# Optimization experiments

Hardware: AMD Instinct MI355X
Metric: run time of the kernel (lower is better)

The kernel has to match this reference:

```python
import jax, jax.numpy as jnp
import numpy as np
import math

EMBED_DIM = 512
B, H, W = 32, 56, 56


def gen_offsets(c):
    # Faithful port of SpiralFC.gen_offset. offset_groups == c (one (dy, dx) pair
    # per input channel). Only pairs 0..c//2-1 are written by the original code
    # (the loop over num_dims writes the same indices twice); the remaining pairs
    # come from torch.empty and are undefined -> we use 0 for determinism.
    dy = np.zeros(c, dtype=np.float32)
    dx = np.zeros(c, dtype=np.float32)
    num_dim = c // 2
    R = 14.0
    for i in range(num_dim):
        if i <= num_dim // 2:
            r = i * (R / num_dim)
        else:
            r = R - i * (R / num_dim)
        dy[i] = round(r * math.cos(math.pi * i / 16))  # torchvision offset order: (y, x)
        dx[i] = round(r * math.sin(math.pi * i / 16))
    return np.stack([dy, dx], axis=1)  # [C, 2]


def setup_inputs() -> dict:
    key = jax.random.key(0)
    k1, k2, k3 = jax.random.split(key, 3)
    C = EMBED_DIM
    fan_in = C  # 1x1 kernel, groups=1
    x = jax.random.normal(k1, (B, H, W, C), dtype=jnp.float32)
    weight = jax.random.normal(k2, (C, C), dtype=jnp.float32) / np.sqrt(fan_in)
    bias = (jax.random.uniform(k3, (C,), dtype=jnp.float32) - 0.5) * (2.0 / np.sqrt(fan_in))
    offset = jnp.asarray(gen_offsets(C))  # [C, 2] fixed buffer
    return {"x": x, "weight": weight, "bias": bias, "offset": offset}


def _shift_bilinear(xc, dy, dx):
    # xc: [B, C, H, W]; dy, dx: [C] spatially-constant per-channel offsets.
    # Bilinear sampling at (h + dy[c], w + dx[c]) with zero padding, separable
    # along H and W because offsets are constant over space.
    Bn, C, Hn, Wn = xc.shape

    def axis_interp(a, off, axis, size):
        p = jnp.arange(size, dtype=off.dtype)[None, :] + off[:, None]  # [C, size]
        p0 = jnp.floor(p)
        w1 = p - p0                      # [C, size]
        i0 = p0.astype(jnp.int32)
        i1 = i0 + 1

        def gather(idx):
            valid = (idx >= 0) & (idx < size)        # [C, size]
            idxc = jnp.clip(idx, 0, size - 1)
            if axis == 2:
                ind = idxc[None, :, :, None]
                msk = valid[None, :, :, None]
            else:
                ind = idxc[None, :, None, :]
                msk = valid[None, :, None, :]
            return jnp.take_along_axis(a, ind, axis=axis) * msk

        if axis == 2:
            w1b = w1[None, :, :, None]
        else:
            w1b = w1[None, :, None, :]
        return gather(i0) * (1.0 - w1b) + gather(i1) * w1b

    xh = axis_interp(xc, dy, 2, Hn)
    return axis_interp(xh, dx, 3, Wn)


def reference(x, weight, bias, offset):
    # x: [B, H, W, C] (NHWC as in SpiralFC.forward)
    xt = jnp.transpose(x, (0, 3, 1, 2))            # [B, C, H, W]
    xs = _shift_bilinear(xt, offset[:, 0], offset[:, 1])
    out = jnp.einsum('bchw,oc->bohw', xs, weight) + bias[None, :, None, None]
    return out  # [B, C, H, W], matching deform_conv2d output layout
```

## Files before the change

### kernel.cpp

```cpp
#include <hip/hip_runtime.h>
#include <hip/hip_bf16.h>


#define HD 56
#define WD 56
#define HW 3136
#define CCH 512
#define NBATCH 32
#define MTOT (NBATCH * HW)

#define BM 128
#define BN 128
#define BK 64

#define XS_ELEMS ((size_t)MTOT * CCH)
#define XS_BYTES (XS_ELEMS * 2)
#define WB_BYTES ((size_t)CCH * CCH * 2)

typedef __attribute__((ext_vector_type(8))) __bf16 bf16x8;
typedef __attribute__((ext_vector_type(4))) float f32x4;
typedef __attribute__((ext_vector_type(8))) unsigned short ushort8_t;

#define AS1 __attribute__((address_space(1)))
#define AS3 __attribute__((address_space(3)))

__device__ __forceinline__ unsigned short f2bf(float f) {
    __hip_bfloat16 h = __float2bfloat16(f);
    return __builtin_bit_cast(unsigned short, h);
}

__device__ __forceinline__ void load16_lds(const unsigned short* g, unsigned short* l) {
    __builtin_amdgcn_global_load_lds((const AS1 unsigned int*)g,
                                     (AS3 unsigned int*)l, 16, 0, 0);
}

#define PIX_BLOCKS (MTOT * (CCH / 8) / 256)
#define WGT_BLOCKS (CCH * CCH / 8 / 256)

__global__ __launch_bounds__(256) void shift_kernel(
    const float* __restrict__ x,
    const float* __restrict__ wgt,
    const float* __restrict__ offs,
    unsigned short* __restrict__ Xs,
    unsigned short* __restrict__ Wb)
{
    const int tid = threadIdx.x;

    if (blockIdx.x >= PIX_BLOCKS) {
        const int e = (blockIdx.x - PIX_BLOCKS) * 256 + tid;
        const float4* src = (const float4*)wgt + (size_t)e * 2;
        float4 a = src[0], b = src[1];
        ushort8_t o;
        o[0] = f2bf(a.x); o[1] = f2bf(a.y); o[2] = f2bf(a.z); o[3] = f2bf(a.w);
        o[4] = f2bf(b.x); o[5] = f2bf(b.y); o[6] = f2bf(b.z); o[7] = f2bf(b.w);
        *(ushort8_t*)(Wb + (size_t)e * 8) = o;
        return;
    }

    const int bid = (int)blockIdx.x;
    const int lb  = (bid & 7) * (PIX_BLOCKS / 8) + (bid >> 3);

    __shared__ int cDy[CCH], cDx[CCH];
    __shared__ int sDy[64], sDx[64], sUni[64];

    for (int k = tid; k < CCH; k += 256) {
        cDy[k] = (int)offs[2 * k];
        cDx[k] = (int)offs[2 * k + 1];
    }
    __syncthreads();
    if (tid < 64) {
        const int c0 = tid * 8;
        int dy = cDy[c0], dx = cDx[c0], u = 1;
#pragma unroll
        for (int j = 1; j < 8; j++)
            u &= (cDy[c0 + j] == dy) & (cDx[c0 + j] == dx);
        sDy[tid] = dy; sDx[tid] = dx; sUni[tid] = u;
    }
    __syncthreads();

    const int e = lb * 256 + tid;
    const int m = e >> 6;
    const int cq = e & 63;
    const int c0 = cq * 8;
    const int b = m / HW;
    const int p = m - b * HW;
    const int y = p / WD;
    const int xx = p - y * WD;

    ushort8_t o = (ushort8_t)0;
    if (sUni[cq]) {
        const int yy = y + sDy[cq];
        const int xs = xx + sDx[cq];
        if ((unsigned)yy < (unsigned)HD && (unsigned)xs < (unsigned)WD) {
            const float4* s = (const float4*)(x + ((size_t)b * HW + yy * WD + xs) * CCH + c0);
            float4 a = s[0], bb = s[1];
            o[0] = f2bf(a.x);  o[1] = f2bf(a.y);  o[2] = f2bf(a.z);  o[3] = f2bf(a.w);
            o[4] = f2bf(bb.x); o[5] = f2bf(bb.y); o[6] = f2bf(bb.z); o[7] = f2bf(bb.w);
        }
    } else {
#pragma unroll
        for (int j = 0; j < 8; j++) {
            const int c = c0 + j;
            const int yy = y + cDy[c];
            const int xs = xx + cDx[c];
            float v = 0.0f;
            if ((unsigned)yy < (unsigned)HD && (unsigned)xs < (unsigned)WD)
                v = x[((size_t)b * HW + yy * WD + xs) * CCH + c];
            o[j] = f2bf(v);
        }
    }
    *(ushort8_t*)(Xs + (size_t)m * CCH + c0) = o;
}

__global__ __launch_bounds__(256) void gemm_kernel(
    const unsigned short* __restrict__ Xs,
    const unsigned short* __restrict__ Wb,
    const float* __restrict__ bias,
    float* __restrict__ out)
{
    __shared__ unsigned short sW[BM * BK];
    __shared__ unsigned short sX[BN * BK];
    __shared__ float sBias[BM];

    const int tid = threadIdx.x;
    const int bid0 = (int)blockIdx.x;
    const int bid  = (bid0 & 7) * (3136 / 8) + (bid0 >> 3);
    const int ot = bid & 3;
    const int pt = bid >> 2;
    const int O0 = ot * BM;
    const int P0 = pt * BN;

    if (tid < BM) sBias[tid] = bias[O0 + tid];

    const int w   = tid >> 6;
    const int l   = tid & 63;
    const int q   = l >> 4;
    const int c16 = l & 15;
    const int wo  = w & 1;
    const int wm  = w >> 1;

    const int lc    = (l & 7) ^ ((l >> 3) & 7);
    const int k7    = c16 & 7;
    const int slot0 = q ^ k7;
    const int slot1 = (4 + q) ^ k7;

    f32x4 acc[4][4];
#pragma unroll
    for (int i = 0; i < 4; i++)
#pragma unroll
        for (int j = 0; j < 4; j++) acc[i][j] = (f32x4)0.0f;

    for (int kk = 0; kk < CCH; kk += BK) {
#pragma unroll
        for (int i = 0; i < 4; i++) {
            const int ib = w * 4 + i;
            const int row = ib * 8 + (l >> 3);
            const unsigned short* gW = Wb + (size_t)(O0 + row) * CCH + kk + lc * 8;
            const unsigned short* gX = Xs + (size_t)(P0 + row) * CCH + kk + lc * 8;
            load16_lds(gW, &sW[ib * 512]);
            load16_lds(gX, &sX[ib * 512]);
        }
        __syncthreads();

#pragma unroll
        for (int s = 0; s < 2; s++) {
            const int slot = s ? slot1 : slot0;
            bf16x8 af[4], bf[4];
#pragma unroll
            for (int i = 0; i < 4; i++) {
                const int row = wo * 64 + i * 16 + c16;
                af[i] = *(const bf16x8*)&sW[row * BK + slot * 8];
            }
#pragma unroll
            for (int j = 0; j < 4; j++) {
                const int row = wm * 64 + j * 16 + c16;
                bf[j] = *(const bf16x8*)&sX[row * BK + slot * 8];
            }
#pragma unroll
            for (int i = 0; i < 4; i++)
#pragma unroll
                for (int j = 0; j < 4; j++)
                    acc[i][j] = __builtin_amdgcn_mfma_f32_16x16x32_bf16(
                        af[i], bf[j], acc[i][j], 0, 0, 0);
        }
        __syncthreads();
    }

#pragma unroll
    for (int j = 0; j < 4; j++) {
        const int g = P0 + wm * 64 + j * 16 + c16;
        const int b = g / HW;
        const int p = g - b * HW;
        float* obase = out + (size_t)b * CCH * HW + p;
#pragma unroll
        for (int i = 0; i < 4; i++) {
#pragma unroll
            for (int r = 0; r < 4; r++) {
                const int o_l = wo * 64 + i * 16 + q * 4 + r;
                obase[(size_t)(O0 + o_l) * HW] = acc[i][j][r] + sBias[o_l];
            }
        }
    }
}

#define LDK 72
__global__ __launch_bounds__(256) void spiralfc_fused(
    const float* __restrict__ x, const float* __restrict__ wgt,
    const float* __restrict__ bias, const float* __restrict__ offs,
    float* __restrict__ out)
{
    __shared__ unsigned short sW[BM * LDK];
    __shared__ unsigned short sX[BN * LDK];
    __shared__ int sDy[CCH];
    __shared__ int sDx[CCH];
    __shared__ float sBias[BM];

    const int tid = threadIdx.x;
    const int bid = blockIdx.x;
    const int O0 = (bid & 3) * BM;
    const int P0 = (bid >> 2) * BN;

    for (int k = tid; k < CCH; k += 256) {
        sDy[k] = (int)offs[2 * k];
        sDx[k] = (int)offs[2 * k + 1];
    }
    if (tid < BM) sBias[tid] = bias[O0 + tid];

    const int w = tid >> 6, l = tid & 63, q = l >> 4, c16 = l & 15;
    const int wo = w & 1, wm = w >> 1;

    f32x4 acc[4][4];
#pragma unroll
    for (int i = 0; i < 4; i++)
#pragma unroll
        for (int j = 0; j < 4; j++) acc[i][j] = (f32x4)0.0f;

    const int kcW = tid & 15, orW = tid >> 4;
    __syncthreads();

    for (int kk = 0; kk < CCH; kk += BK) {
#pragma unroll
        for (int ps = 0; ps < 8; ps++) {
            const int o = ps * 16 + orW;
            const float4 wv = *(const float4*)(wgt + (size_t)(O0 + o) * CCH + kk + kcW * 4);
            ushort4 uv;
            uv.x = f2bf(wv.x); uv.y = f2bf(wv.y); uv.z = f2bf(wv.z); uv.w = f2bf(wv.w);
            *(ushort4*)&sW[o * LDK + kcW * 4] = uv;
        }
#pragma unroll 4
        for (int ps = 0; ps < 32; ps++) {
            const int m = ps * 4 + w;
            const int g = P0 + m;
            const int b = g / HW;
            const int p = g - b * HW;
            const int y = p / WD;
            const int xx = p - y * WD;
            const int k = kk + l;
            const int yy = y + sDy[k];
            const int xs = xx + sDx[k];
            float v = 0.0f;
            if ((unsigned)yy < (unsigned)HD && (unsigned)xs < (unsigned)WD)
                v = x[((size_t)b * HW + yy * WD + xs) * CCH + k];
            sX[m * LDK + l] = f2bf(v);
        }
        __syncthreads();
#pragma unroll
        for (int s = 0; s < 2; s++) {
            bf16x8 af[4], bf[4];
#pragma unroll
            for (int i = 0; i < 4; i++)
                af[i] = *(const bf16x8*)&sW[(wo * 64 + i * 16 + c16) * LDK + s * 32 + q * 8];
#pragma unroll
            for (int j = 0; j < 4; j++)
                bf[j] = *(const bf16x8*)&sX[(wm * 64 + j * 16 + c16) * LDK + s * 32 + q * 8];
#pragma unroll
            for (int i = 0; i < 4; i++)
#pragma unroll
                for (int j = 0; j < 4; j++)
                    acc[i][j] = __builtin_amdgcn_mfma_f32_16x16x32_bf16(
                        af[i], bf[j], acc[i][j], 0, 0, 0);
        }
        __syncthreads();
    }
#pragma unroll
    for (int j = 0; j < 4; j++) {
        const int g = P0 + wm * 64 + j * 16 + c16;
        const int b = g / HW;
        const int p = g - b * HW;
        float* obase = out + (size_t)b * CCH * HW + p;
#pragma unroll
        for (int i = 0; i < 4; i++)
#pragma unroll
            for (int r = 0; r < 4; r++) {
                const int o_l = wo * 64 + i * 16 + q * 4 + r;
                obase[(size_t)(O0 + o_l) * HW] = acc[i][j][r] + sBias[o_l];
            }
    }
}

extern "C" void kernel_launch(void* const* d_in, const int* in_sizes, int n_in,
                              void* d_out, int out_size, void* d_ws, size_t ws_size,
                              hipStream_t stream) {
    const float* x    = (const float*)d_in[0];
    const float* wgt  = (const float*)d_in[1];
    const float* bias = (const float*)d_in[2];
    const float* offs = (const float*)d_in[3];
    float* out = (float*)d_out;

    if (ws_size >= XS_BYTES + WB_BYTES) {
        unsigned short* Xs = (unsigned short*)d_ws;
        unsigned short* Wb = (unsigned short*)((char*)d_ws + XS_BYTES);
        shift_kernel<<<dim3(PIX_BLOCKS + WGT_BLOCKS), dim3(256), 0, stream>>>(
            x, wgt, offs, Xs, Wb);
        gemm_kernel<<<dim3(3136), dim3(256), 0, stream>>>(Xs, Wb, bias, out);
    } else {
        spiralfc_fused<<<dim3(3136), dim3(256), 0, stream>>>(x, wgt, bias, offs, out);
    }
}
```

Baseline: 515.4 us.

## Rewrite shift kernel as scatter over padded pixel tiles with per-channel threads

The shift pre-pass now assigns one thread per channel and walks 64 consecutive source pixels, scattering each bf16 value to its shifted destination row instead of gathering 8-channel vectors per destination pixel. Offsets are read directly per channel, so the shared-memory uniformity table and the divergent per-channel gather path are gone. A padding of 448 pixels on each end covers every shift magnitude. In exchange, global stores become 2-byte scattered writes per thread rather than 16-byte vector stores, which may raise write-transaction cost.

```diff
diff --git a/kernel.cpp b/kernel.cpp
--- a/kernel.cpp
+++ b/kernel.cpp
@@ -34,10 +34,13 @@
                                      (AS3 unsigned int*)l, 16, 0, 0);
 }
 
-#define PIX_BLOCKS (MTOT * (CCH / 8) / 256)
+#define TILE 64
+#define SPAD 448
+#define NTILES ((MTOT + 2 * SPAD) / TILE)
+#define SHIFT_BLOCKS (NTILES * 2)
 #define WGT_BLOCKS (CCH * CCH / 8 / 256)
 
-__global__ __launch_bounds__(256) void shift_kernel(
+__global__ __launch_bounds__(256) void shift_t_kernel(
     const float* __restrict__ x,
     const float* __restrict__ wgt,
     const float* __restrict__ offs,
@@ -45,9 +48,10 @@
     unsigned short* __restrict__ Wb)
 {
     const int tid = threadIdx.x;
-
-    if (blockIdx.x >= PIX_BLOCKS) {
-        const int e = (blockIdx.x - PIX_BLOCKS) * 256 + tid;
+    const int bid0 = (int)blockIdx.x;
+
+    if (bid0 >= SHIFT_BLOCKS) {
+        const int e = (bid0 - SHIFT_BLOCKS) * 256 + tid;
         const float4* src = (const float4*)wgt + (size_t)e * 2;
         float4 a = src[0], b = src[1];
         ushort8_t o;
@@ -57,59 +61,47 @@
         return;
     }
 
-    const int bid = (int)blockIdx.x;
-    const int lb  = (bid & 7) * (PIX_BLOCKS / 8) + (bid >> 3);
-
-    __shared__ int cDy[CCH], cDx[CCH];
-    __shared__ int sDy[64], sDx[64], sUni[64];
-
-    for (int k = tid; k < CCH; k += 256) {
-        cDy[k] = (int)offs[2 * k];
-        cDx[k] = (int)offs[2 * k + 1];
-    }
-    __syncthreads();
-    if (tid < 64) {
-        const int c0 = tid * 8;
-        int dy = cDy[c0], dx = cDx[c0], u = 1;
-#pragma unroll
-        for (int j = 1; j < 8; j++)
-            u &= (cDy[c0 + j] == dy) & (cDx[c0 + j] == dx);
-        sDy[tid] = dy; sDx[tid] = dx; sUni[tid] = u;
-    }
-    __syncthreads();
-
-    const int e = lb * 256 + tid;
-    const int m = e >> 6;
-    const int cq = e & 63;
-    const int c0 = cq * 8;
-    const int b = m / HW;
-    const int p = m - b * HW;
-    const int y = p / WD;
-    const int xx = p - y * WD;
-
-    ushort8_t o = (ushort8_t)0;
-    if (sUni[cq]) {
-        const int yy = y + sDy[cq];
-        const int xs = xx + sDx[cq];
-        if ((unsigned)yy < (unsigned)HD && (unsigned)xs < (unsigned)WD) {
-            const float4* s = (const float4*)(x + ((size_t)b * HW + yy * WD + xs) * CCH + c0);
-            float4 a = s[0], bb = s[1];
-            o[0] = f2bf(a.x);  o[1] = f2bf(a.y);  o[2] = f2bf(a.z);  o[3] = f2bf(a.w);
-            o[4] = f2bf(bb.x); o[5] = f2bf(bb.y); o[6] = f2bf(bb.z); o[7] = f2bf(bb.w);
-        }
-    } else {
-#pragma unroll
-        for (int j = 0; j < 8; j++) {
-            const int c = c0 + j;
-            const int yy = y + cDy[c];
-            const int xs = xx + cDx[c];
-            float v = 0.0f;
-            if ((unsigned)yy < (unsigned)HD && (unsigned)xs < (unsigned)WD)
-                v = x[((size_t)b * HW + yy * WD + xs) * CCH + c];
-            o[j] = f2bf(v);
-        }
-    }
-    *(ushort8_t*)(Xs + (size_t)m * CCH + c0) = o;
+    const int nq = SHIFT_BLOCKS / 8, nr = SHIFT_BLOCKS % 8;
+    const int xcd = bid0 & 7;
+    const int bid = (xcd < nr ? xcd * (nq + 1) : nr * (nq + 1) + (xcd - nr) * nq)
+                    + (bid0 >> 3);
+
+    const int tile = bid >> 1;
+    const int half = bid & 1;
+    const int c = half * 256 + tid;
+    const int i0 = tile * TILE - SPAD;
+
+    const int dy = (int)offs[2 * c];
+    const int dx = (int)offs[2 * c + 1];
+    const int s  = dy * WD + dx;
+
+    const int mm = i0 + HW;
+    const int pp = mm % HW;
+    int yi = pp / WD;
+    int xi = pp - yi * WD;
+
+#pragma unroll
+    for (int pb = 0; pb < 4; pb++) {
+        float v[16];
+#pragma unroll
+        for (int t = 0; t < 16; t++) {
+            const int p = pb * 16 + t;
+            const unsigned ui = (unsigned)(i0 + p);
+            v[t] = (ui < (unsigned)MTOT) ? x[(size_t)ui * CCH + c] : 0.0f;
+        }
+#pragma unroll
+        for (int t = 0; t < 16; t++) {
+            const int p = pb * 16 + t;
+            const bool valid = ((unsigned)(xi - dx) < (unsigned)WD) &
+                               ((unsigned)(yi - dy) < (unsigned)HD);
+            const unsigned short uv = valid ? f2bf(v[t]) : (unsigned short)0;
+            const unsigned um = (unsigned)(i0 + p - s);
+            if (um < (unsigned)MTOT)
+                Xs[(size_t)um * CCH + c] = uv;
+            xi++;
+            if (xi == WD) { xi = 0; yi++; if (yi == HD) yi = 0; }
+        }
+    }
 }
 
 __global__ __launch_bounds__(256) void gemm_kernel(
@@ -310,7 +302,7 @@
     if (ws_size >= XS_BYTES + WB_BYTES) {
         unsigned short* Xs = (unsigned short*)d_ws;
         unsigned short* Wb = (unsigned short*)((char*)d_ws + XS_BYTES);
-        shift_kernel<<<dim3(PIX_BLOCKS + WGT_BLOCKS), dim3(256), 0, stream>>>(
+        shift_t_kernel<<<dim3(SHIFT_BLOCKS + WGT_BLOCKS), dim3(256), 0, stream>>>(
             x, wgt, offs, Xs, Wb);
         gemm_kernel<<<dim3(3136), dim3(256), 0, stream>>>(Xs, Wb, bias, out);
     } else {
```

After: 682.4 us. 1.32x slower.
